# Kernel tuning notes

Measured on AMD Instinct MI355X. Metric: run time of the kernel, lower is better.

The kernel has to match this reference:

```python
import jax, jax.numpy as jnp
from jax import lax
import numpy as np

IN_SIZE, H_SIZE, OUT_SIZE, SEAS = 48, 128, 48, 24
DILATIONS = (1, 2, 4, 8)  # cells 0-1 = DRNN group 0, cells 2-3 = DRNN group 1


def setup_inputs() -> dict:
    key = jax.random.key(0)
    ks = jax.random.split(key, 16)
    B, T = 256, 512
    inp = {
        'train': jax.random.uniform(ks[0], (B, T), jnp.float32, 0.5, 1.5),
        'val': jax.random.uniform(ks[1], (B, OUT_SIZE), jnp.float32, 0.5, 1.5),
        'test': jax.random.uniform(ks[2], (B, OUT_SIZE), jnp.float32, 0.5, 1.5),
        'init_lev_sm': jnp.array([0.5], jnp.float32),
        'init_seas_sm': jnp.array([0.5], jnp.float32),
        'init_seasonalities': jnp.full((SEAS,), 0.5, jnp.float32),
    }
    cin = [IN_SIZE, H_SIZE, H_SIZE, H_SIZE]
    k = 3
    for i in range(4):
        inp[f'w_ih{i}'] = jax.random.normal(ks[k], (4 * H_SIZE, cin[i]), jnp.float32) * 0.05; k += 1
        inp[f'w_hh{i}'] = jax.random.normal(ks[k], (4 * H_SIZE, H_SIZE), jnp.float32) * 0.05; k += 1
        inp[f'b_ih{i}'] = jnp.zeros((4 * H_SIZE,), jnp.float32)
        inp[f'b_hh{i}'] = jnp.zeros((4 * H_SIZE,), jnp.float32)
    inp['nl_w'] = jax.random.normal(ks[k], (H_SIZE, H_SIZE), jnp.float32) * 0.05; k += 1
    inp['nl_b'] = jnp.zeros((H_SIZE,), jnp.float32)
    inp['sc_w'] = jax.random.normal(ks[k], (OUT_SIZE, H_SIZE), jnp.float32) * 0.05; k += 1
    inp['sc_b'] = jnp.zeros((OUT_SIZE,), jnp.float32)
    return inp


def _lstm(x, w_ih, w_hh, b_ih, b_hh):
    # x: (T, N, C) -> (T, N, H); torch LSTM gate order i, f, g, o
    n, h = x.shape[1], w_hh.shape[1]

    def step(carry, xt):
        hp, cp = carry
        g = xt @ w_ih.T + hp @ w_hh.T + (b_ih + b_hh)
        i, f, gg, o = jnp.split(g, 4, axis=-1)
        c = jax.nn.sigmoid(f) * cp + jax.nn.sigmoid(i) * jnp.tanh(gg)
        hn = jax.nn.sigmoid(o) * jnp.tanh(c)
        return (hn, c), hn

    z = jnp.zeros((n, h), x.dtype)
    _, hs = lax.scan(step, (z, z), x)
    return hs


def _dilated_lstm(x, d, w_ih, w_hh, b_ih, b_hh):
    # DRNN dilation: fold time by d into batch, run cell, unfold
    t, b, c = x.shape
    td = -(-t // d) * d
    xp = jnp.pad(x, ((0, td - t), (0, 0), (0, 0)))
    xd = xp.reshape(td // d, d, b, c).reshape(td // d, d * b, c)
    out = _lstm(xd, w_ih, w_hh, b_ih, b_hh)
    h = out.shape[-1]
    return out.reshape(td // d, d, b, h).reshape(td, b, h)[:t]


def _series_forward(data, cells, nl_w, nl_b, sc_w, sc_b):
    # ResidualDRNN: group 0 (cells 0,1), group 1 (cells 2,3) with residual add
    x = data
    for grp in range(2):
        res = x
        for ci in (2 * grp, 2 * grp + 1):
            x = _dilated_lstm(x, DILATIONS[ci], *cells[ci])
        if grp > 0:
            x = x + res
    x = jnp.tanh(x @ nl_w.T + nl_b)
    return x @ sc_w.T + sc_b


def _esrnn(train, val, init_lev_sm, init_seas_sm, init_seasonalities, cells, nl_w, nl_b, sc_w, sc_b):
    B, T = train.shape
    lev_sm = jax.nn.sigmoid(init_lev_sm[0])
    seas_sm = jax.nn.sigmoid(init_seas_sm[0])
    s0 = jnp.exp(init_seasonalities)  # (SEAS,) shared across series
    lev0 = train[:, 0] / s0[0]  # (B,)
    # rolling buffer: at step i it holds seasonalities[i .. i+SEAS-1]
    buf0 = jnp.broadcast_to(jnp.concatenate([s0[1:], s0[:1]])[:, None], (SEAS, B))

    def step(carry, x_t):
        lev_p, buf = carry
        seas_t = buf[0]
        lev_n = lev_sm * (x_t / seas_t) + (1 - lev_sm) * lev_p
        seas_n = seas_sm * (x_t / lev_n) + (1 - seas_sm) * seas_t
        return (lev_n, jnp.concatenate([buf[1:], seas_n[None]], 0)), (lev_n, seas_n)

    _, (levs_r, seas_r) = lax.scan(step, (lev0, buf0), train[:, 1:].T)
    levs = jnp.concatenate([lev0[None], levs_r], 0).T  # (B, T)
    seas_head = jnp.broadcast_to(jnp.concatenate([s0, s0[:1]])[:, None], (SEAS + 1, B))
    seas = jnp.concatenate([seas_head, seas_r], 0).T  # (B, T+SEAS)
    if OUT_SIZE > SEAS:  # seasonality extension branch
        start = seas.shape[1] - SEAS
        seas = jnp.concatenate([seas, seas[:, start:start + OUT_SIZE - SEAS]], 1)
    W = T - IN_SIZE + 1
    Wo = T - OUT_SIZE - IN_SIZE + 1
    idx_in = jnp.arange(W)[:, None] + jnp.arange(IN_SIZE)[None, :]  # (W, IN)
    win_in = (train[:, idx_in] / seas[:, idx_in] / levs[:, IN_SIZE - 1:, None]).transpose(1, 0, 2)  # (W,B,IN)
    idx_out = jnp.arange(Wo)[:, None] + IN_SIZE + jnp.arange(OUT_SIZE)[None, :]
    win_out = (train[:, idx_out] / seas[:, idx_out] / levs[:, IN_SIZE - 1:IN_SIZE - 1 + Wo, None]).transpose(1, 0, 2)
    network_pred = _series_forward(win_in[:-OUT_SIZE], cells, nl_w, nl_b, sc_w, sc_b)  # (Wo,B,OUT)
    network_act = win_out
    net_out_all = _series_forward(win_in, cells, nl_w, nl_b, sc_w, sc_b)  # (W,B,OUT)
    hold = net_out_all[-1] * seas[:, -OUT_SIZE:] * levs[:, -1:]
    hold_out_pred = hold * (hold > 0).astype(hold.dtype)
    hold_out_act = val  # testing=False path
    hold_out_act_norm = val / seas[:, -OUT_SIZE:] / levs[:, -1:]
    return network_pred, network_act, hold_out_pred, net_out_all, hold_out_act, hold_out_act_norm


def reference(train, val, test, init_lev_sm, init_seas_sm, init_seasonalities,
              w_ih0, w_hh0, b_ih0, b_hh0, w_ih1, w_hh1, b_ih1, b_hh1,
              w_ih2, w_hh2, b_ih2, b_hh2, w_ih3, w_hh3, b_ih3, b_hh3,
              nl_w, nl_b, sc_w, sc_b):
    cells = ((w_ih0, w_hh0, b_ih0, b_hh0), (w_ih1, w_hh1, b_ih1, b_hh1),
             (w_ih2, w_hh2, b_ih2, b_hh2), (w_ih3, w_hh3, b_ih3, b_hh3))
    return _esrnn(train, val, init_lev_sm, init_seas_sm, init_seasonalities,
                  cells, nl_w, nl_b, sc_w, sc_b)
```

## Files before the change

### kernel.cpp

```cpp
#include <hip/hip_runtime.h>
#include <cstdint>
#include <cstddef>

typedef _Float16 half8 __attribute__((ext_vector_type(8)));
typedef _Float16 half4 __attribute__((ext_vector_type(4)));
typedef float floatx4 __attribute__((ext_vector_type(4)));

namespace {
constexpr int kB = 256, kT = 512, kIN = 48, kOUT = 48, kSEAS = 24, kH = 128;
constexpr int kW = kT - kIN + 1;
constexpr int kWO = kT - kOUT - kIN + 1;
constexpr int kNB = kW * kB;
constexpr int kMBLK = kNB / 16;
constexpr float kLOG2E = 1.44269504088896340736f;
}

#if __has_builtin(__builtin_amdgcn_exp2f)
#define FEXP2(x) __builtin_amdgcn_exp2f(x)
#else
#define FEXP2(x) exp2f(x)
#endif
#if __has_builtin(__builtin_amdgcn_rcpf)
#define FRCP(x) __builtin_amdgcn_rcpf(x)
#else
#define FRCP(x) (1.0f / (x))
#endif

__device__ __forceinline__ float fsig(float y) { return FRCP(1.0f + FEXP2(-y)); }
__device__ __forceinline__ float ftanh(float x) { return 2.0f * fsig(2.0f * kLOG2E * x) - 1.0f; }

__global__ void k_transpose(const float* __restrict__ train, float* __restrict__ trainT) {
  int t = blockIdx.x, b = threadIdx.x;
  trainT[t * kB + b] = train[b * kT + t];
}

__global__ void k_es(const float* __restrict__ trainT, const float* __restrict__ levp,
                     const float* __restrict__ seasp, const float* __restrict__ inits,
                     float* __restrict__ seas, float* __restrict__ levs) {
  __shared__ float ring[kSEAS][kB];
  int b = threadIdx.x;
  float lev_sm = fsig(levp[0] * kLOG2E);
  float seas_sm = fsig(seasp[0] * kLOG2E);
  float s00 = expf(inits[0]);
  for (int s = 0; s < kSEAS; ++s) {
    float v = expf(inits[s]);
    seas[s * kB + b] = v;
    if (s >= 1) ring[s - 1][b] = v;
  }
  ring[kSEAS - 1][b] = s00;
  seas[kSEAS * kB + b] = s00;
  float lev = trainT[b] * FRCP(s00);
  levs[b] = lev;
  int rk = 0;
  float x_nx = trainT[kB + b];
  float st_nx = ring[0][b];
  for (int k = 0; k < kT - 1; ++k) {
    float x = x_nx;
    float st = st_nx;
    if (k + 1 < kT - 1) x_nx = trainT[(k + 2) * kB + b];
    int rn = (rk + 1 == kSEAS) ? 0 : rk + 1;
    st_nx = ring[rn][b];
    float ln = lev_sm * (x * FRCP(st)) + (1.0f - lev_sm) * lev;
    float sn = seas_sm * (x * FRCP(ln)) + (1.0f - seas_sm) * st;
    ring[rk][b] = sn;
    seas[(k + kSEAS + 1) * kB + b] = sn;
    levs[(k + 1) * kB + b] = ln;
    lev = ln;
    rk = rn;
  }
  for (int j = 0; j < kOUT - kSEAS; ++j)
    seas[(kT + kSEAS + j) * kB + b] = seas[(kT + j) * kB + b];
}

__global__ void k_win_in(const float* __restrict__ trainT, const float* __restrict__ seas,
                         const float* __restrict__ levs, _Float16* __restrict__ win) {
  int w = blockIdx.x;
  int tid = threadIdx.x;
#pragma unroll
  for (int i = 0; i < 16; ++i) {
    int o = i * 256 + tid;
    int b = o >> 3;
    int j0 = (o & 7) * 8;
    half8 h;
    if (j0 < kIN) {
      float rl = FRCP(levs[(kIN - 1 + w) * kB + b]);
#pragma unroll
      for (int jj = 0; jj < 8; ++jj) {
        int j = j0 + jj;
        int t = w + j;
        float v = (j < kIN) ? trainT[t * kB + b] * FRCP(seas[t * kB + b]) * rl : 0.0f;
        h[jj] = (_Float16)v;
      }
    } else {
#pragma unroll
      for (int jj = 0; jj < 8; ++jj) h[jj] = (_Float16)0.0f;
    }
    *(half8*)(win + ((size_t)(w * kB + b)) * 64 + j0) = h;
  }
}

__global__ void k_win_out(const float* __restrict__ trainT, const float* __restrict__ seas,
                          const float* __restrict__ levs, float* __restrict__ out1) {
  int idx = blockIdx.x * 256 + threadIdx.x;
  if (idx >= kWO * kB * (kOUT / 4)) return;
  int row = idx / 12;
  int j0 = (idx - row * 12) * 4;
  int wo = row >> 8;
  int b = row & 255;
  float rl = FRCP(levs[(kIN - 1 + wo) * kB + b]);
  floatx4 v;
#pragma unroll
  for (int jj = 0; jj < 4; ++jj) {
    int t = kIN + wo + j0 + jj;
    v[jj] = trainT[t * kB + b] * FRCP(seas[t * kB + b]) * rl;
  }
  *(floatx4*)(out1 + (size_t)row * kOUT + j0) = v;
}

__device__ __forceinline__ void prep_bias_elem(const float* bih, const float* bhh, float* dst,
                                               int c) {
  int ct = c >> 4, n16 = c & 15, g = ct & 3, wv = ct >> 2;
  int row = g * 128 + wv * 16 + n16;
  float sc = (g == 2) ? 2.0f * kLOG2E : kLOG2E;
  dst[c] = (bih[row] + bhh[row]) * sc;
}

__device__ __forceinline__ void prep_frag_elem(const float* Wsrc, _Float16* dst, int KB, int Kreal,
                                               int srcld, int perm, int idx) {
  int jj = idx & 7;
  int lane = (idx >> 3) & 63;
  int kb = (idx >> 9) % KB;
  int ct = idx / (KB * 512);
  int n16 = lane & 15;
  int k = kb * 32 + ((lane >> 4) << 3) + jj;
  int row;
  float sc;
  if (perm) {
    int g = ct & 3, wv = ct >> 2;
    row = g * 128 + wv * 16 + n16;
    sc = (g == 2) ? 2.0f * kLOG2E : kLOG2E;
  } else {
    row = ct * 16 + n16;
    sc = 1.0f;
  }
  float v = (k < Kreal) ? Wsrc[row * srcld + k] * sc : 0.0f;
  dst[idx] = (_Float16)v;
}

struct PrepArgs {
  const float* bih[4];
  const float* bhh[4];
  float* biasp[4];
  const float* wih[4];
  _Float16* wihf[4];
  const float* whh[4];
  _Float16* whhf[4];
  const float* nlw;
  _Float16* nlf;
  const float* scw;
  _Float16* scf;
};

__global__ void k_prep_all(PrepArgs a) {
  int seg = blockIdx.y;
  int idx = blockIdx.x * 256 + threadIdx.x;
  if (seg < 4) {
    if (idx < 512) prep_bias_elem(a.bih[seg], a.bhh[seg], a.biasp[seg], idx);
  } else if (seg == 4) {
    if (idx < 32 * 2 * 512) prep_frag_elem(a.wih[0], a.wihf[0], 2, 48, 48, 1, idx);
  } else if (seg < 8) {
    int c = seg - 4;
    if (idx < 32 * 4 * 512) prep_frag_elem(a.wih[c], a.wihf[c], 4, 128, 128, 1, idx);
  } else if (seg < 12) {
    int c = seg - 8;
    if (idx < 32 * 4 * 512) prep_frag_elem(a.whh[c], a.whhf[c], 4, 128, 128, 1, idx);
  } else if (seg == 12) {
    if (idx < 8 * 4 * 512) prep_frag_elem(a.nlw, a.nlf, 4, 128, 128, 0, idx);
  } else {
    if (idx < 3 * 4 * 512) prep_frag_elem(a.scw, a.scf, 4, 128, 128, 0, idx);
  }
}

__global__ void k_zero_prog(int* prog) {
  int i = threadIdx.x;
  if (i < 192) prog[i] = 0;
}

template <int NT, int KB, int MODE>
__global__ __launch_bounds__(512) void k_gemm(const _Float16* __restrict__ A,
                                              const _Float16* __restrict__ A2, int Khalfs,
                                              const _Float16* __restrict__ Bfr,
                                              const float* __restrict__ bias,
                                              _Float16* __restrict__ outh,
                                              float* __restrict__ outf,
                                              float* __restrict__ outf2) {
  __shared__ _Float16 bsh[NT * KB * 512];
  int tid = threadIdx.x;
  {
    const uint4* src = (const uint4*)Bfr;
    uint4* dst = (uint4*)bsh;
    for (int i = tid; i < NT * KB * 64; i += 512) dst[i] = src[i];
  }
  __syncthreads();
  int wv = tid >> 6, lane = tid & 63;
  int mblk = blockIdx.x * 8 + wv;
  if (mblk >= kMBLK) return;
  int m = lane & 15, kq = lane >> 4;
  const _Float16* arow = A + (size_t)(mblk * 16 + m) * Khalfs + kq * 8;
  half8 af[KB];
#pragma unroll
  for (int kb = 0; kb < KB; ++kb) af[kb] = *(const half8*)(arow + kb * 32);
  if constexpr (MODE == 1) {
    const _Float16* arow2 = A2 + (size_t)(mblk * 16 + m) * Khalfs + kq * 8;
#pragma unroll
    for (int kb = 0; kb < KB; ++kb) {
      half8 a2 = *(const half8*)(arow2 + kb * 32);
      af[kb] += a2;
    }
  }
#pragma unroll
  for (int t0 = 0; t0 < NT; t0 += 2) {
    float b0 = bias[t0 * 16 + m];
    floatx4 acc0 = {b0, b0, b0, b0};
    floatx4 acc1 = {0.f, 0.f, 0.f, 0.f};
    if (t0 + 1 < NT) {
      float b1 = bias[(t0 + 1) * 16 + m];
      acc1 = (floatx4){b1, b1, b1, b1};
    }
#pragma unroll
    for (int kb = 0; kb < KB; ++kb) {
      half8 bf0 = *(const half8*)(&bsh[((t0 * KB + kb) * 64 + lane) * 8]);
      acc0 = __builtin_amdgcn_mfma_f32_16x16x32_f16(af[kb], bf0, acc0, 0, 0, 0);
      if (t0 + 1 < NT) {
        half8 bf1 = *(const half8*)(&bsh[(((t0 + 1) * KB + kb) * 64 + lane) * 8]);
        acc1 = __builtin_amdgcn_mfma_f32_16x16x32_f16(af[kb], bf1, acc1, 0, 0, 0);
      }
    }
    if constexpr (MODE == 1) {
#pragma unroll
      for (int r = 0; r < 4; ++r) {
        int row = mblk * 16 + kq * 4 + r;
        outh[(size_t)row * kH + t0 * 16 + m] = (_Float16)ftanh(acc0[r]);
        if (t0 + 1 < NT) outh[(size_t)row * kH + (t0 + 1) * 16 + m] = (_Float16)ftanh(acc1[r]);
      }
    } else {
#pragma unroll
      for (int r = 0; r < 4; ++r) {
        int row = mblk * 16 + kq * 4 + r;
        float v0 = acc0[r];
        outf[(size_t)row * kOUT + t0 * 16 + m] = v0;
        if (row < kWO * kB) outf2[(size_t)row * kOUT + t0 * 16 + m] = v0;
        if (t0 + 1 < NT) {
          float v1 = acc1[r];
          outf[(size_t)row * kOUT + (t0 + 1) * 16 + m] = v1;
          if (row < kWO * kB) outf2[(size_t)row * kOUT + (t0 + 1) * 16 + m] = v1;
        }
      }
    }
  }
}

struct FArgs {
  const _Float16* win;
  const _Float16* wihf[4];
  const _Float16* whhf[4];
  const float* biasp[4];
  _Float16* H[4];
  int* prog;
};

__device__ __forceinline__ void wait_prog(int* p, int need, int& fenced, int* obs_sh) {
  if (need <= fenced) return;
  if (threadIdx.x == 0) {
    int v;
    while ((v = __hip_atomic_load(p, __ATOMIC_RELAXED, __HIP_MEMORY_SCOPE_AGENT)) < need)
      __builtin_amdgcn_s_sleep(16);
    *obs_sh = v;
  }
  __syncthreads();
  int v = *obs_sh;
  __builtin_amdgcn_fence(__ATOMIC_ACQUIRE, "agent");
  fenced = v;
}

template <int KXB, bool POLL, bool REL>
__device__ __forceinline__ void floop(const _Float16* __restrict__ Xsrc,
                                      const _Float16* __restrict__ wihp,
                                      const _Float16* __restrict__ whhp,
                                      const float* __restrict__ bp, _Float16* __restrict__ Hout,
                                      int* progIn, int sprev, int* progOut, int d, int kd, int ib,
                                      _Float16 (*hbuf)[2048], int* obs_sh) {
  int tid = threadIdx.x;
  int wv = tid >> 6, lane = tid & 63, m = lane & 15, kq = lane >> 4;
  half8 wxf[4][KXB], whf[4][4];
#pragma unroll
  for (int g = 0; g < 4; ++g) {
#pragma unroll
    for (int kb = 0; kb < KXB; ++kb)
      wxf[g][kb] = *(const half8*)(wihp + ((((wv * 4 + g) * KXB + kb) * 64 + lane) * 8));
#pragma unroll
    for (int kb = 0; kb < 4; ++kb)
      whf[g][kb] = *(const half8*)(whhp + ((((wv * 4 + g) * 4 + kb) * 64 + lane) * 8));
  }
  float bg[4];
#pragma unroll
  for (int g = 0; g < 4; ++g) bg[g] = bp[(wv * 4 + g) * 16 + m];
  float cc[4] = {0.f, 0.f, 0.f, 0.f};
  int nsteps = (kW - kd + d - 1) / d;
  const int xstride = KXB * 32;
  int fenced = 0;
  if (POLL) wait_prog(progIn + (kd & ((1 << sprev) - 1)), (kd >> sprev) + 1, fenced, obs_sh);
  half8 hxc[KXB], hxn[KXB];
  {
    const _Float16* xr = Xsrc + (size_t)(kd * kB + ib * 16 + m) * xstride + kq * 8;
#pragma unroll
    for (int kb = 0; kb < KXB; ++kb) hxc[kb] = *(const half8*)(xr + kb * 32);
  }
  for (int j = 0; j < nsteps; ++j) {
    int ph = j & 1;
    int wtn = (j + 1) * d + kd;
    bool havenext = (j + 1 < nsteps);
    if (POLL && havenext)
      wait_prog(progIn + (wtn & ((1 << sprev) - 1)), (wtn >> sprev) + 1, fenced, obs_sh);
    floatx4 acc[4];
#pragma unroll
    for (int g = 0; g < 4; ++g) acc[g] = (floatx4){bg[g], bg[g], bg[g], bg[g]};
    if (havenext) {
      const _Float16* xr = Xsrc + (size_t)(wtn * kB + ib * 16 + m) * xstride + kq * 8;
#pragma unroll
      for (int kb = 0; kb < KXB; ++kb) hxn[kb] = *(const half8*)(xr + kb * 32);
    }
#pragma unroll
    for (int kb = 0; kb < KXB; ++kb)
#pragma unroll
      for (int g = 0; g < 4; ++g)
        acc[g] = __builtin_amdgcn_mfma_f32_16x16x32_f16(hxc[kb], wxf[g][kb], acc[g], 0, 0, 0);
    if (j > 0) {
#pragma unroll
      for (int kb = 0; kb < 4; ++kb) {
        int gran = (kb * 4 + kq) ^ m;
        half8 a = *(const half8*)(&hbuf[ph ^ 1][m * 128 + gran * 8]);
#pragma unroll
        for (int g = 0; g < 4; ++g)
          acc[g] = __builtin_amdgcn_mfma_f32_16x16x32_f16(a, whf[g][kb], acc[g], 0, 0, 0);
      }
    }
#pragma unroll
    for (int r = 0; r < 4; ++r) {
      float iv = fsig(acc[0][r]);
      float fv = fsig(acc[1][r]);
      float g2 = fsig(acc[2][r]);
      float ov = fsig(acc[3][r]);
      cc[r] = fv * cc[r] + iv * (2.0f * g2 - 1.0f);
      float tc = 2.0f * fsig(cc[r] * (2.0f * kLOG2E)) - 1.0f;
      float hv = ov * tc;
      int brow = kq * 4 + r;
      int hu = wv * 16 + m;
      int gran = (hu >> 3) ^ brow;
      hbuf[ph][brow * 128 + gran * 8 + (hu & 7)] = (_Float16)hv;
    }
    __syncthreads();
    {
      int hr = tid >> 5, hu0 = (tid & 31) * 4;
      int gran = (hu0 >> 3) ^ hr;
      half4 hv4 = *(const half4*)(&hbuf[ph][hr * 128 + gran * 8 + (hu0 & 7)]);
      *(half4*)(Hout + (size_t)((j * d + kd) * kB + ib * 16 + hr) * kH + hu0) = hv4;
    }
    if (REL && (((j & 7) == 7) || (j + 1 == nsteps))) {
      __syncthreads();
      if (tid == 0)
        __hip_atomic_store(progOut, j + 1, __ATOMIC_RELEASE, __HIP_MEMORY_SCOPE_AGENT);
    }
#pragma unroll
    for (int kb = 0; kb < KXB; ++kb) hxc[kb] = hxn[kb];
  }
}

__global__ __launch_bounds__(512) void k_fused(FArgs a) {
  __shared__ _Float16 hbuf[2][2048];
  __shared__ int obs_sh;
  int w = blockIdx.x;
  int cell, d, kd, ib;
  if (w < 16) {
    cell = 0; d = 1; kd = 0; ib = w;
  } else if (w < 48) {
    cell = 1; d = 2; kd = (w - 16) >> 4; ib = (w - 16) & 15;
  } else if (w < 112) {
    cell = 2; d = 4; kd = (w - 48) >> 4; ib = (w - 48) & 15;
  } else {
    cell = 3; d = 8; kd = (w - 112) >> 4; ib = (w - 112) & 15;
  }
  const _Float16* Xsrc = (cell == 0) ? a.win : a.H[cell - 1];
  _Float16* Hout = a.H[cell];
  int* progOut = a.prog + (cell * 16 + ib) * 4 + kd;
  int* progIn = (cell > 0) ? a.prog + ((cell - 1) * 16 + ib) * 4 : nullptr;
  int sprev = (cell == 2) ? 1 : ((cell == 3) ? 2 : 0);
  if (cell == 0)
    floop<2, false, true>(Xsrc, a.wihf[0], a.whhf[0], a.biasp[0], Hout, nullptr, 0, progOut, d,
                          kd, ib, hbuf, &obs_sh);
  else if (cell < 3)
    floop<4, true, true>(Xsrc, a.wihf[cell], a.whhf[cell], a.biasp[cell], Hout, progIn, sprev,
                         progOut, d, kd, ib, hbuf, &obs_sh);
  else
    floop<4, true, false>(Xsrc, a.wihf[3], a.whhf[3], a.biasp[3], Hout, progIn, sprev, progOut,
                          d, kd, ib, hbuf, &obs_sh);
}

__global__ void k_tail(const float* __restrict__ out3, const float* __restrict__ val,
                       const float* __restrict__ seas, const float* __restrict__ levs,
                       float* __restrict__ out2, float* __restrict__ out4,
                       float* __restrict__ out5) {
  int idx = blockIdx.x * 256 + threadIdx.x;
  int b = idx / kOUT, j = idx % kOUT;
  float s = seas[(kT + j) * kB + b];
  float L = levs[(kT - 1) * kB + b];
  float net = out3[(size_t)(kW - 1) * kB * kOUT + idx];
  float hp = net * s * L;
  out2[idx] = hp > 0.0f ? hp : 0.0f;
  float v = val[idx];
  out4[idx] = v;
  out5[idx] = v / s / L;
}

extern "C" void kernel_launch(void* const* d_in, const int* in_sizes, int n_in, void* d_out,
                              int out_size, void* d_ws, size_t ws_size, hipStream_t stream) {
  const float* train = (const float*)d_in[0];
  const float* val = (const float*)d_in[1];
  const float* levp = (const float*)d_in[3];
  const float* seasp = (const float*)d_in[4];
  const float* inits = (const float*)d_in[5];
  const float* w_ih[4] = {(const float*)d_in[6], (const float*)d_in[10], (const float*)d_in[14],
                          (const float*)d_in[18]};
  const float* w_hh[4] = {(const float*)d_in[7], (const float*)d_in[11], (const float*)d_in[15],
                          (const float*)d_in[19]};
  const float* b_ih[4] = {(const float*)d_in[8], (const float*)d_in[12], (const float*)d_in[16],
                          (const float*)d_in[20]};
  const float* b_hh[4] = {(const float*)d_in[9], (const float*)d_in[13], (const float*)d_in[17],
                          (const float*)d_in[21]};
  const float* nl_w = (const float*)d_in[22];
  const float* nl_b = (const float*)d_in[23];
  const float* sc_w = (const float*)d_in[24];
  const float* sc_b = (const float*)d_in[25];

  char* wsb = (char*)d_ws;
  size_t off = 0;
  auto alloc = [&](size_t bytes) -> void* {
    void* p = wsb + off;
    off = (off + bytes + 255) & ~(size_t)255;
    return p;
  };
  float* trainT = (float*)alloc((size_t)kT * kB * 4);
  float* seas = (float*)alloc((size_t)560 * kB * 4);
  float* levs = (float*)alloc((size_t)kT * kB * 4);
  _Float16* win = (_Float16*)alloc((size_t)kNB * 64 * 2);
  _Float16* Hc[4];
  for (int c = 0; c < 4; ++c) Hc[c] = (_Float16*)alloc((size_t)kNB * kH * 2);
  _Float16* U = (_Float16*)alloc((size_t)kNB * kH * 2);
  float* biasp[4];
  for (int c = 0; c < 4; ++c) biasp[c] = (float*)alloc(512 * 4);
  _Float16* wihf[4];
  wihf[0] = (_Float16*)alloc((size_t)32 * 2 * 512 * 2);
  for (int c = 1; c < 4; ++c) wihf[c] = (_Float16*)alloc((size_t)32 * 4 * 512 * 2);
  _Float16* whhf[4];
  for (int c = 0; c < 4; ++c) whhf[c] = (_Float16*)alloc((size_t)32 * 4 * 512 * 2);
  _Float16* nlf = (_Float16*)alloc((size_t)8 * 4 * 512 * 2);
  _Float16* scf = (_Float16*)alloc((size_t)3 * 4 * 512 * 2);
  int* prog = (int*)alloc(192 * 4);

  float* out0 = (float*)d_out;
  float* out1 = out0 + (size_t)kWO * kB * kOUT;
  float* out2 = out1 + (size_t)kWO * kB * kOUT;
  float* out3 = out2 + (size_t)kB * kOUT;
  float* out4 = out3 + (size_t)kW * kB * kOUT;
  float* out5 = out4 + (size_t)kB * kOUT;

  k_transpose<<<kT, kB, 0, stream>>>(train, trainT);
  k_es<<<1, kB, 0, stream>>>(trainT, levp, seasp, inits, seas, levs);
  k_win_in<<<kW, kB, 0, stream>>>(trainT, seas, levs, win);
  k_win_out<<<(kWO * kB * 12 + 255) / 256, 256, 0, stream>>>(trainT, seas, levs, out1);

  PrepArgs pa;
  for (int c = 0; c < 4; ++c) {
    pa.bih[c] = b_ih[c]; pa.bhh[c] = b_hh[c]; pa.biasp[c] = biasp[c];
    pa.wih[c] = w_ih[c]; pa.wihf[c] = wihf[c];
    pa.whh[c] = w_hh[c]; pa.whhf[c] = whhf[c];
  }
  pa.nlw = nl_w; pa.nlf = nlf; pa.scw = sc_w; pa.scf = scf;
  k_prep_all<<<dim3(256, 14), 256, 0, stream>>>(pa);
  k_zero_prog<<<1, 256, 0, stream>>>(prog);

  FArgs fa;
  fa.win = win;
  for (int c = 0; c < 4; ++c) {
    fa.wihf[c] = wihf[c]; fa.whhf[c] = whhf[c]; fa.biasp[c] = biasp[c]; fa.H[c] = Hc[c];
  }
  fa.prog = prog;
  void* kp[1] = {(void*)&fa};
  hipLaunchCooperativeKernel((void*)k_fused, dim3(240), dim3(512), kp, 0, stream);

  const int GG = kMBLK / 8;
  k_gemm<8, 4, 1><<<GG, 512, 0, stream>>>(Hc[3], Hc[1], 128, nlf, nl_b, U, nullptr, nullptr);
  k_gemm<3, 4, 2><<<GG, 512, 0, stream>>>(U, nullptr, 128, scf, sc_b, nullptr, out3, out0);
  k_tail<<<48, 256, 0, stream>>>(out3, val, seas, levs, out2, out4, out5);
}
```

Before: 712.3 us.

## Restructure ES recurrence into register blocks and precompute deseasonalized ratios

The exponential smoothing kernel now keeps the 24 seasonal values in registers and processes the recurrence in blocks of 24 steps. Loads are batched and reciprocals of seasonality are computed ahead of the serial level chain. It also stores x/seas as a ratio array that the window kernels read, which removes a reciprocal and a second load per element there. The LSTM output store now writes half scalars straight from registers instead of staging through LDS. That trades coalesced half4 stores for strided 2-byte stores and adds an extra workspace buffer.

```diff
diff --git a/kernel.cpp b/kernel.cpp
--- a/kernel.cpp
+++ b/kernel.cpp
@@ -34,46 +34,66 @@
   trainT[t * kB + b] = train[b * kT + t];
 }
 
+template <int N>
+__device__ __forceinline__ void es_block(int k0, int b, float lev_sm, float omb_l,
+                                         float seas_sm, float omb_s, float& lev,
+                                         float (&stprev)[kSEAS],
+                                         const float* __restrict__ trainT,
+                                         float* __restrict__ seas, float* __restrict__ levs,
+                                         float* __restrict__ ratio) {
+  float x[N], q[N], lv[N];
+#pragma unroll
+  for (int jj = 0; jj < N; ++jj) x[jj] = trainT[(k0 + jj + 1) * kB + b];
+#pragma unroll
+  for (int jj = 0; jj < N; ++jj) q[jj] = x[jj] * FRCP(stprev[jj]);
+#pragma unroll
+  for (int jj = 0; jj < N; ++jj) {
+    lev = lev_sm * q[jj] + omb_l * lev;
+    lv[jj] = lev;
+  }
+#pragma unroll
+  for (int jj = 0; jj < N; ++jj) {
+    float sn = seas_sm * (x[jj] * FRCP(lv[jj])) + omb_s * stprev[jj];
+    stprev[jj] = sn;
+    seas[(k0 + jj + kSEAS + 1) * kB + b] = sn;
+    levs[(k0 + jj + 1) * kB + b] = lv[jj];
+    ratio[(k0 + jj + 1) * kB + b] = q[jj];
+  }
+}
+
 __global__ void k_es(const float* __restrict__ trainT, const float* __restrict__ levp,
                      const float* __restrict__ seasp, const float* __restrict__ inits,
-                     float* __restrict__ seas, float* __restrict__ levs) {
-  __shared__ float ring[kSEAS][kB];
+                     float* __restrict__ seas, float* __restrict__ levs,
+                     float* __restrict__ ratio) {
   int b = threadIdx.x;
   float lev_sm = fsig(levp[0] * kLOG2E);
   float seas_sm = fsig(seasp[0] * kLOG2E);
+  float omb_l = 1.0f - lev_sm, omb_s = 1.0f - seas_sm;
+  float stprev[kSEAS];
   float s00 = expf(inits[0]);
+#pragma unroll
   for (int s = 0; s < kSEAS; ++s) {
     float v = expf(inits[s]);
     seas[s * kB + b] = v;
-    if (s >= 1) ring[s - 1][b] = v;
-  }
-  ring[kSEAS - 1][b] = s00;
+    if (s >= 1) stprev[s - 1] = v;
+  }
+  stprev[kSEAS - 1] = s00;
   seas[kSEAS * kB + b] = s00;
   float lev = trainT[b] * FRCP(s00);
   levs[b] = lev;
-  int rk = 0;
-  float x_nx = trainT[kB + b];
-  float st_nx = ring[0][b];
-  for (int k = 0; k < kT - 1; ++k) {
-    float x = x_nx;
-    float st = st_nx;
-    if (k + 1 < kT - 1) x_nx = trainT[(k + 2) * kB + b];
-    int rn = (rk + 1 == kSEAS) ? 0 : rk + 1;
-    st_nx = ring[rn][b];
-    float ln = lev_sm * (x * FRCP(st)) + (1.0f - lev_sm) * lev;
-    float sn = seas_sm * (x * FRCP(ln)) + (1.0f - seas_sm) * st;
-    ring[rk][b] = sn;
-    seas[(k + kSEAS + 1) * kB + b] = sn;
-    levs[(k + 1) * kB + b] = ln;
-    lev = ln;
-    rk = rn;
-  }
+  ratio[b] = lev;
+#pragma unroll 1
+  for (int blk = 0; blk < 21; ++blk)
+    es_block<24>(blk * kSEAS, b, lev_sm, omb_l, seas_sm, omb_s, lev, stprev, trainT, seas,
+                 levs, ratio);
+  es_block<7>(504, b, lev_sm, omb_l, seas_sm, omb_s, lev, stprev, trainT, seas, levs,
+              ratio);
   for (int j = 0; j < kOUT - kSEAS; ++j)
     seas[(kT + kSEAS + j) * kB + b] = seas[(kT + j) * kB + b];
 }
 
-__global__ void k_win_in(const float* __restrict__ trainT, const float* __restrict__ seas,
-                         const float* __restrict__ levs, _Float16* __restrict__ win) {
+__global__ void k_win_in(const float* __restrict__ ratio, const float* __restrict__ levs,
+                         _Float16* __restrict__ win) {
   int w = blockIdx.x;
   int tid = threadIdx.x;
 #pragma unroll
@@ -87,8 +107,7 @@
 #pragma unroll
       for (int jj = 0; jj < 8; ++jj) {
         int j = j0 + jj;
-        int t = w + j;
-        float v = (j < kIN) ? trainT[t * kB + b] * FRCP(seas[t * kB + b]) * rl : 0.0f;
+        float v = (j < kIN) ? ratio[(w + j) * kB + b] * rl : 0.0f;
         h[jj] = (_Float16)v;
       }
     } else {
@@ -99,8 +118,8 @@
   }
 }
 
-__global__ void k_win_out(const float* __restrict__ trainT, const float* __restrict__ seas,
-                          const float* __restrict__ levs, float* __restrict__ out1) {
+__global__ void k_win_out(const float* __restrict__ ratio, const float* __restrict__ levs,
+                          float* __restrict__ out1) {
   int idx = blockIdx.x * 256 + threadIdx.x;
   if (idx >= kWO * kB * (kOUT / 4)) return;
   int row = idx / 12;
@@ -110,10 +129,7 @@
   float rl = FRCP(levs[(kIN - 1 + wo) * kB + b]);
   floatx4 v;
 #pragma unroll
-  for (int jj = 0; jj < 4; ++jj) {
-    int t = kIN + wo + j0 + jj;
-    v[jj] = trainT[t * kB + b] * FRCP(seas[t * kB + b]) * rl;
-  }
+  for (int jj = 0; jj < 4; ++jj) v[jj] = ratio[(kIN + wo + j0 + jj) * kB + b] * rl;
   *(floatx4*)(out1 + (size_t)row * kOUT + j0) = v;
 }
 
@@ -182,8 +198,7 @@
 }
 
 __global__ void k_zero_prog(int* prog) {
-  int i = threadIdx.x;
-  if (i < 192) prog[i] = 0;
+  prog[threadIdx.x] = 0;
 }
 
 template <int NT, int KB, int MODE>
@@ -312,9 +327,9 @@
   if (POLL) wait_prog(progIn + (kd & ((1 << sprev) - 1)), (kd >> sprev) + 1, fenced, obs_sh);
   half8 hxc[KXB], hxn[KXB];
   {
-    const _Float16* xr = Xsrc + (size_t)(kd * kB + ib * 16 + m) * xstride + kq * 8;
-#pragma unroll
-    for (int kb = 0; kb < KXB; ++kb) hxc[kb] = *(const half8*)(xr + kb * 32);
+    const _Float16* xrow = Xsrc + (size_t)(kd * kB + ib * 16 + m) * xstride + kq * 8;
+#pragma unroll
+    for (int kb = 0; kb < KXB; ++kb) hxc[kb] = *(const half8*)(xrow + kb * 32);
   }
   for (int j = 0; j < nsteps; ++j) {
     int ph = j & 1;
@@ -326,9 +341,9 @@
 #pragma unroll
     for (int g = 0; g < 4; ++g) acc[g] = (floatx4){bg[g], bg[g], bg[g], bg[g]};
     if (havenext) {
-      const _Float16* xr = Xsrc + (size_t)(wtn * kB + ib * 16 + m) * xstride + kq * 8;
-#pragma unroll
-      for (int kb = 0; kb < KXB; ++kb) hxn[kb] = *(const half8*)(xr + kb * 32);
+      const _Float16* xrow = Xsrc + (size_t)(wtn * kB + ib * 16 + m) * xstride + kq * 8;
+#pragma unroll
+      for (int kb = 0; kb < KXB; ++kb) hxn[kb] = *(const half8*)(xrow + kb * 32);
     }
 #pragma unroll
     for (int kb = 0; kb < KXB; ++kb)
@@ -345,6 +360,7 @@
           acc[g] = __builtin_amdgcn_mfma_f32_16x16x32_f16(a, whf[g][kb], acc[g], 0, 0, 0);
       }
     }
+    _Float16 hv[4];
 #pragma unroll
     for (int r = 0; r < 4; ++r) {
       float iv = fsig(acc[0][r]);
@@ -353,18 +369,18 @@
       float ov = fsig(acc[3][r]);
       cc[r] = fv * cc[r] + iv * (2.0f * g2 - 1.0f);
       float tc = 2.0f * fsig(cc[r] * (2.0f * kLOG2E)) - 1.0f;
-      float hv = ov * tc;
+      hv[r] = (_Float16)(ov * tc);
       int brow = kq * 4 + r;
       int hu = wv * 16 + m;
       int gran = (hu >> 3) ^ brow;
-      hbuf[ph][brow * 128 + gran * 8 + (hu & 7)] = (_Float16)hv;
+      hbuf[ph][brow * 128 + gran * 8 + (hu & 7)] = hv[r];
     }
     __syncthreads();
     {
-      int hr = tid >> 5, hu0 = (tid & 31) * 4;
-      int gran = (hu0 >> 3) ^ hr;
-      half4 hv4 = *(const half4*)(&hbuf[ph][hr * 128 + gran * 8 + (hu0 & 7)]);
-      *(half4*)(Hout + (size_t)((j * d + kd) * kB + ib * 16 + hr) * kH + hu0) = hv4;
+      int hu = wv * 16 + m;
+      size_t rb = (size_t)((j * d + kd) * kB + ib * 16 + kq * 4);
+#pragma unroll
+      for (int r = 0; r < 4; ++r) Hout[(rb + r) * kH + hu] = hv[r];
     }
     if (REL && (((j & 7) == 7) || (j + 1 == nsteps))) {
       __syncthreads();
@@ -452,6 +468,7 @@
   float* trainT = (float*)alloc((size_t)kT * kB * 4);
   float* seas = (float*)alloc((size_t)560 * kB * 4);
   float* levs = (float*)alloc((size_t)kT * kB * 4);
+  float* ratio = (float*)alloc((size_t)kT * kB * 4);
   _Float16* win = (_Float16*)alloc((size_t)kNB * 64 * 2);
   _Float16* Hc[4];
   for (int c = 0; c < 4; ++c) Hc[c] = (_Float16*)alloc((size_t)kNB * kH * 2);
@@ -465,7 +482,7 @@
   for (int c = 0; c < 4; ++c) whhf[c] = (_Float16*)alloc((size_t)32 * 4 * 512 * 2);
   _Float16* nlf = (_Float16*)alloc((size_t)8 * 4 * 512 * 2);
   _Float16* scf = (_Float16*)alloc((size_t)3 * 4 * 512 * 2);
-  int* prog = (int*)alloc(192 * 4);
+  int* prog = (int*)alloc(256 * 4);
 
   float* out0 = (float*)d_out;
   float* out1 = out0 + (size_t)kWO * kB * kOUT;
@@ -475,9 +492,9 @@
   float* out5 = out4 + (size_t)kB * kOUT;
 
   k_transpose<<<kT, kB, 0, stream>>>(train, trainT);
-  k_es<<<1, kB, 0, stream>>>(trainT, levp, seasp, inits, seas, levs);
-  k_win_in<<<kW, kB, 0, stream>>>(trainT, seas, levs, win);
-  k_win_out<<<(kWO * kB * 12 + 255) / 256, 256, 0, stream>>>(trainT, seas, levs, out1);
+  k_es<<<1, kB, 0, stream>>>(trainT, levp, seasp, inits, seas, levs, ratio);
+  k_win_in<<<kW, kB, 0, stream>>>(ratio, levs, win);
+  k_win_out<<<(kWO * kB * 12 + 255) / 256, 256, 0, stream>>>(ratio, levs, out1);
 
   PrepArgs pa;
   for (int c = 0; c < 4; ++c) {
```

After: 687.8 us. 1.04x faster.
